# Performance work log

Measured on AMD Instinct MI355X. Metric: run time of the kernel, lower is better.

Reference implementation:

```python
import jax, jax.numpy as jnp
import numpy as np

N, NFEAT, NHID, NHEADS, NCLASS = 4096, 1024, 128, 8, 64
ALPHA = 0.2  # LeakyReLU negative slope
NEG_INF = -9e15


def setup_inputs() -> dict:
    key = jax.random.key(0)
    ks = jax.random.split(key, 8)
    x = jax.random.normal(ks[0], (N, NFEAT), dtype=jnp.float32)
    adj = jax.random.randint(ks[1], (N, N), 0, 2, dtype=jnp.int32)
    sW = 1.0 / np.sqrt(NFEAT)
    W = jax.random.normal(ks[2], (NHEADS, NFEAT, NHID), dtype=jnp.float32) * sW
    a1 = jax.random.normal(ks[3], (NHEADS, NHID), dtype=jnp.float32) * 0.1
    a2 = jax.random.normal(ks[4], (NHEADS, NHID), dtype=jnp.float32) * 0.1
    sWo = 1.0 / np.sqrt(NHID * NHEADS)
    Wo = jax.random.normal(ks[5], (NHID * NHEADS, NCLASS), dtype=jnp.float32) * sWo
    ao1 = jax.random.normal(ks[6], (NCLASS,), dtype=jnp.float32) * 0.1
    ao2 = jax.random.normal(ks[7], (NCLASS,), dtype=jnp.float32) * 0.1
    return {"x": x, "adj": adj, "W": W, "a1": a1, "a2": a2,
            "Wo": Wo, "ao1": ao1, "ao2": ao2}


def reference(x, adj, W, a1, a2, Wo, ao1, ao2):
    mask = adj > 0  # [N, N]
    # --- multi-head attention layer (concat=True) ---
    Wh = jnp.einsum('nf,hfd->hnd', x, W)            # [H, N, D]
    f1 = jnp.einsum('hnd,hd->hn', Wh, a1)           # [H, N] self score
    f2 = jnp.einsum('hnd,hd->hn', Wh, a2)           # [H, N] neighbor score
    e = jax.nn.leaky_relu(f1[:, :, None] + f2[:, None, :], negative_slope=ALPHA)
    e = jnp.where(mask[None, :, :], e, NEG_INF)
    attn = jax.nn.softmax(e, axis=-1)               # [H, N, N]
    h = jnp.einsum('hnm,hmd->hnd', attn, Wh)        # [H, N, D]
    h = jax.nn.elu(h)                               # concat=True applies elu
    h = jnp.transpose(h, (1, 0, 2)).reshape(N, NHEADS * NHID)  # concat heads
    # --- output attention layer (concat=False) ---
    Who = h @ Wo                                    # [N, C]
    g1 = Who @ ao1                                  # [N]
    g2 = Who @ ao2                                  # [N]
    eo = jax.nn.leaky_relu(g1[:, None] + g2[None, :], negative_slope=ALPHA)
    eo = jnp.where(mask, eo, NEG_INF)
    ao = jax.nn.softmax(eo, axis=-1)                # [N, N]
    out = ao @ Who                                  # [N, C]
    out = jax.nn.elu(out)                           # F.elu in GAT.forward
    return jax.nn.log_softmax(out, axis=1)
```

## Files before the change

### kernel.cpp

```cpp
#include <hip/hip_runtime.h>
#include <hip/hip_bf16.h>


#define NN    4096
#define NF    1024
#define DH    128
#define NHEADS 8
#define NCLS  64
#define ALPHA 0.2f
#define LOG2E 1.44269504f

using short8 = __attribute__((ext_vector_type(8))) short;
using f32x4  = __attribute__((ext_vector_type(4))) float;
using int4v  = __attribute__((ext_vector_type(4))) int;

static __device__ __forceinline__ float bf2f(unsigned short h) {
    return __uint_as_float(((unsigned int)h) << 16);
}
static __device__ __forceinline__ unsigned short f2bf(float f) {
    unsigned int u = __float_as_uint(f);
    u = (u + 0x7fffu + ((u >> 16) & 1u)) >> 16;
    return (unsigned short)u;
}
static __device__ __forceinline__ float fast_exp2(float x) {
    return __builtin_amdgcn_exp2f(x);
}

__global__ __launch_bounds__(256) void diag_fill(
    float* __restrict__ out, int n, float val)
{
    int i = blockIdx.x * 256 + threadIdx.x;
    if (i < n) out[i] = val;
}

__global__ __launch_bounds__(256) void convert_misc(
    const float* __restrict__ x, const float* __restrict__ a1,
    const float* __restrict__ a2, const float* __restrict__ ao1,
    const float* __restrict__ ao2, unsigned short* __restrict__ xB,
    unsigned short* __restrict__ a1B, unsigned short* __restrict__ a2B,
    unsigned short* __restrict__ ao1B, unsigned short* __restrict__ ao2B)
{
    int b = blockIdx.x, t = threadIdx.x;
    if (b < 4096) {
        long i = ((long)b * 256 + t) * 4;
        float4 v = *(const float4*)&x[i];
        unsigned u0 = (unsigned)f2bf(v.x) | ((unsigned)f2bf(v.y) << 16);
        unsigned u1 = (unsigned)f2bf(v.z) | ((unsigned)f2bf(v.w) << 16);
        uint2 u; u.x = u0; u.y = u1;
        *(uint2*)&xB[i] = u;
    } else if (b == 4096) {
        for (int i = t; i < NHEADS * DH; i += 256) {
            a1B[i] = f2bf(a1[i]);
            a2B[i] = f2bf(a2[i]);
        }
    } else {
        if (t < NCLS) {
            ao1B[t] = f2bf(ao1[t]);
            ao2B[t] = f2bf(ao2[t]);
        }
    }
}

__global__ __launch_bounds__(256) void transpose_cvt(
    const float* __restrict__ W, const float* __restrict__ Wo,
    unsigned short* __restrict__ WT, unsigned short* __restrict__ WoT)
{
    __shared__ unsigned short tile[32][33];
    int z = blockIdx.z;
    const float* in; unsigned short* out; int C;
    if (z < 8) { in = W + (long)z * NF * DH; out = WT + (long)z * DH * NF; C = DH; }
    else       { in = Wo;                    out = WoT;                    C = NCLS; }
    int x0 = blockIdx.x * 32, y0 = blockIdx.y * 32;
    if (x0 >= C) return;
    int t = threadIdx.x, tx = t & 31, ty = t >> 5;
    for (int yy = 0; yy < 32; yy += 8)
        tile[ty + yy][tx] = f2bf(in[(long)(y0 + ty + yy) * C + x0 + tx]);
    __syncthreads();
    for (int yy = 0; yy < 32; yy += 8)
        out[(long)(x0 + ty + yy) * NF + y0 + tx] = tile[tx][ty + yy];
}

__global__ __launch_bounds__(256) void build_mask(
    const int* __restrict__ adj, unsigned int* __restrict__ bm)
{
    long t4 = (long)blockIdx.x * 256 + threadIdx.x;
    int4v v = ((const int4v*)adj)[t4];
    unsigned nib = (v[0] > 0 ? 1u : 0u) | (v[1] > 0 ? 2u : 0u)
                 | (v[2] > 0 ? 4u : 0u) | (v[3] > 0 ? 8u : 0u);
    int l = threadIdx.x & 63;
    unsigned w = nib << (4 * (l & 7));
    w |= __shfl_xor(w, 1);
    w |= __shfl_xor(w, 2);
    w |= __shfl_xor(w, 4);
    if ((l & 7) == 0) bm[t4 >> 3] = w;
}

__global__ __launch_bounds__(256) void gemm_bt(
    const unsigned short* __restrict__ A, const unsigned short* __restrict__ Bt,
    unsigned short* __restrict__ Cc, int K, int Nn, long sAz, long sCz)
{
    __shared__ unsigned short Alds[64][72];
    __shared__ unsigned short Blds[128][72];
    int t = threadIdx.x;
    int w = t >> 6, l = t & 63;
    long aoff = (long)blockIdx.z * sAz + (long)blockIdx.y * 64 * K;
    long boff = (long)blockIdx.x * 128 * K;
    f32x4 acc[8];
#pragma unroll
    for (int i = 0; i < 8; ++i) acc[i] = (f32x4){0.f, 0.f, 0.f, 0.f};

    for (int k0 = 0; k0 < K; k0 += 64) {
#pragma unroll
        for (int it = 0; it < 2; ++it) {
            int ci = it * 256 + t;
            int r = ci >> 3, c8 = (ci & 7) * 8;
            *(short8*)&Alds[r][c8] = *(const short8*)&A[aoff + (long)r * K + k0 + c8];
        }
#pragma unroll
        for (int it = 0; it < 4; ++it) {
            int ci = it * 256 + t;
            int r = ci >> 3, c8 = (ci & 7) * 8;
            *(short8*)&Blds[r][c8] = *(const short8*)&Bt[boff + (long)r * K + k0 + c8];
        }
        __syncthreads();
        int arow = w * 16 + (l & 15);
        int koff = (l >> 4) * 8;
#pragma unroll
        for (int kc = 0; kc < 2; ++kc) {
            short8 af = *(const short8*)&Alds[arow][kc * 32 + koff];
#pragma unroll
            for (int dt = 0; dt < 8; ++dt) {
                short8 bf = *(const short8*)&Blds[dt * 16 + (l & 15)][kc * 32 + koff];
                acc[dt] = __builtin_amdgcn_mfma_f32_16x16x32_bf16(af, bf, acc[dt], 0, 0, 0);
            }
        }
        __syncthreads();
    }
    long coff = (long)blockIdx.z * sCz + ((long)blockIdx.y * 64) * Nn + blockIdx.x * 128;
    int mrow = w * 16 + (l >> 4) * 4;
#pragma unroll
    for (int dt = 0; dt < 8; ++dt) {
        int n = dt * 16 + (l & 15);
#pragma unroll
        for (int r = 0; r < 4; ++r)
            Cc[coff + (long)(mrow + r) * Nn + n] = f2bf(acc[dt][r]);
    }
}

__global__ __launch_bounds__(256) void gemm2_ks(
    const unsigned short* __restrict__ A, const unsigned short* __restrict__ Bt,
    float* __restrict__ accw, int K, int kchunk)
{
    __shared__ unsigned short Alds[64][72];
    __shared__ unsigned short Blds[128][72];
    int t = threadIdx.x;
    int w = t >> 6, l = t & 63;
    long boff = (long)blockIdx.x * 128 * K;
    int kz = blockIdx.z;
    f32x4 acc[8];
#pragma unroll
    for (int i = 0; i < 8; ++i) acc[i] = (f32x4){0.f, 0.f, 0.f, 0.f};

    for (int k0 = kz * kchunk; k0 < (kz + 1) * kchunk; k0 += 64) {
#pragma unroll
        for (int it = 0; it < 2; ++it) {
            int ci = it * 256 + t;
            int r = ci >> 3, c8 = (ci & 7) * 8;
            *(short8*)&Alds[r][c8] = *(const short8*)&A[(long)r * K + k0 + c8];
        }
#pragma unroll
        for (int it = 0; it < 4; ++it) {
            int ci = it * 256 + t;
            int r = ci >> 3, c8 = (ci & 7) * 8;
            *(short8*)&Blds[r][c8] = *(const short8*)&Bt[boff + (long)r * K + k0 + c8];
        }
        __syncthreads();
        int arow = w * 16 + (l & 15);
        int koff = (l >> 4) * 8;
#pragma unroll
        for (int kc = 0; kc < 2; ++kc) {
            short8 af = *(const short8*)&Alds[arow][kc * 32 + koff];
#pragma unroll
            for (int dt = 0; dt < 8; ++dt) {
                short8 bf = *(const short8*)&Blds[dt * 16 + (l & 15)][kc * 32 + koff];
                acc[dt] = __builtin_amdgcn_mfma_f32_16x16x32_bf16(af, bf, acc[dt], 0, 0, 0);
            }
        }
        __syncthreads();
    }
    int mrow = w * 16 + (l >> 4) * 4;
#pragma unroll
    for (int dt = 0; dt < 8; ++dt) {
        int n = blockIdx.x * 128 + dt * 16 + (l & 15);
        *(f32x4*)&accw[((long)kz * NN + n) * NCLS + mrow] = acc[dt];
    }
}

__global__ __launch_bounds__(256) void combinew(
    const float* __restrict__ accw, const unsigned short* __restrict__ ao1B,
    const unsigned short* __restrict__ ao2B, unsigned short* __restrict__ WhoT,
    float* __restrict__ g1, float* __restrict__ g2)
{
    int t = threadIdx.x, wv = t >> 6, l = t & 63;
    int n = blockIdx.x * 4 + wv;
    float v = 0.f;
#pragma unroll
    for (int kz = 0; kz < 4; ++kz)
        v += accw[((long)kz * NN + n) * NCLS + l];
    unsigned short b = f2bf(v);
    WhoT[(long)l * NN + n] = b;
    float vf = bf2f(b);
    float s1 = vf * bf2f(ao1B[l]);
    float s2 = vf * bf2f(ao2B[l]);
#pragma unroll
    for (int off = 32; off; off >>= 1) {
        s1 += __shfl_xor(s1, off);
        s2 += __shfl_xor(s2, off);
    }
    if (l == 0) { g1[n] = s1 * LOG2E; g2[n] = s2 * LOG2E; }
}

__global__ __launch_bounds__(256) void fscores(
    const unsigned short* __restrict__ T, const unsigned short* __restrict__ va,
    const unsigned short* __restrict__ vb, float* __restrict__ fa,
    float* __restrict__ fb, int D, int Nn)
{
    int h = blockIdx.y;
    int n = blockIdx.x * 256 + threadIdx.x;
    const unsigned short* Th = T + (long)h * D * Nn;
    float s1 = 0.f, s2 = 0.f;
    for (int d = 0; d < D; ++d) {
        float v = bf2f(Th[(long)d * Nn + n]);
        s1 += v * bf2f(va[h * D + d]);
        s2 += v * bf2f(vb[h * D + d]);
    }
    fa[h * Nn + n] = s1 * LOG2E;
    fb[h * Nn + n] = s2 * LOG2E;
}

static __device__ __forceinline__ float build_p16(
    unsigned int bits, float fi, const float* f2s, int pc0,
    short8& p0, short8& p1)
{
    float lsum = 0.f;
#pragma unroll
    for (int cc = 0; cc < 16; ++cc) {
        float wgt = 0.f;
        if ((bits >> cc) & 1u) {
            float e = fi + f2s[pc0 + cc];
            e = e > 0.f ? e : ALPHA * e;
            e = fminf(e, 60.f);
            wgt = fast_exp2(e);
        }
        unsigned short bw = f2bf(wgt);
        lsum += bf2f(bw);
        if (cc < 8) p0[cc] = (short)bw;
        else        p1[cc - 8] = (short)bw;
    }
    return lsum;
}

static __device__ __forceinline__ void build_pfrag3(
    unsigned long long wpair, float fi, const float* __restrict__ f2g,
    int kgrp, short8& a0, short8& a1)
{
    int4v av0, av1;
#pragma unroll
    for (int kc = 0; kc < 2; ++kc) {
        unsigned bits = (unsigned)(wpair >> (kc * 32 + kgrp * 8)) & 0xFFu;
        const float4* fp = (const float4*)(f2g + kc * 32 + kgrp * 8);
        float4 fv0 = fp[0], fv1 = fp[1];
        float ev[8] = {fv0.x, fv0.y, fv0.z, fv0.w, fv1.x, fv1.y, fv1.z, fv1.w};
#pragma unroll
        for (int jj = 0; jj < 8; jj += 2) {
            float e0 = fi + ev[jj], e1 = fi + ev[jj + 1];
            e0 = fmaxf(e0, ALPHA * e0);
            e1 = fmaxf(e1, ALPHA * e1);
            float w0 = fast_exp2(e0), w1 = fast_exp2(e1);
            w0 = ((bits >> jj) & 1u) ? w0 : 0.f;
            w1 = ((bits >> (jj + 1)) & 1u) ? w1 : 0.f;
            float2 fv; fv.x = w0; fv.y = w1;
            __hip_bfloat162 pk = __float22bfloat162_rn(fv);
            unsigned pu; __builtin_memcpy(&pu, &pk, 4);
            if (kc == 0) av0[jj >> 1] = (int)pu;
            else         av1[jj >> 1] = (int)pu;
        }
    }
    a0 = __builtin_bit_cast(short8, av0);
    a1 = __builtin_bit_cast(short8, av1);
}

__global__ __launch_bounds__(256) void attn1_direct(
    const float* __restrict__ f1, const float* __restrict__ f2,
    const unsigned int* __restrict__ bm, const unsigned short* __restrict__ WhT,
    unsigned short* __restrict__ hcat)
{
    __shared__ unsigned short Plds[64][72];
    __shared__ unsigned short Wlds[128][72];
    __shared__ float f1s[64], f2s[64], ssum[64][4], srow[64];
    int t = threadIdx.x;
    int h = blockIdx.y;
    int i0 = blockIdx.x * 64;
    int w = t >> 6, l = t & 63;
    if (t < 64) f1s[t] = f1[h * NN + i0 + t];
    f32x4 acc[8];
#pragma unroll
    for (int i = 0; i < 8; ++i) acc[i] = (f32x4){0.f, 0.f, 0.f, 0.f};
    float psum = 0.f;
    int pr = t >> 2, pc0 = (t & 3) * 16;
    const unsigned short* Wh_h = WhT + (long)h * DH * NN;

    for (int j0 = 0; j0 < NN; j0 += 64) {
        if (t < 64) f2s[t] = f2[h * NN + j0 + t];
        __syncthreads();
        {
            unsigned int word = bm[(long)(i0 + pr) * (NN / 32) + (j0 >> 5) + ((pc0 >> 5) & 1)];
            unsigned int bits = (word >> (pc0 & 16)) & 0xFFFFu;
            short8 p0, p1;
            psum += build_p16(bits, f1s[pr], f2s, pc0, p0, p1);
            *(short8*)&Plds[pr][pc0]     = p0;
            *(short8*)&Plds[pr][pc0 + 8] = p1;
        }
#pragma unroll
        for (int it = 0; it < 4; ++it) {
            int ci = it * 256 + t;
            int d = ci >> 3, c8 = (ci & 7) * 8;
            *(short8*)&Wlds[d][c8] = *(const short8*)&Wh_h[(long)d * NN + j0 + c8];
        }
        __syncthreads();
        int arow = w * 16 + (l & 15);
        int koff = (l >> 4) * 8;
#pragma unroll
        for (int kc = 0; kc < 2; ++kc) {
            short8 af = *(const short8*)&Plds[arow][kc * 32 + koff];
#pragma unroll
            for (int dt = 0; dt < 8; ++dt) {
                short8 bf = *(const short8*)&Wlds[dt * 16 + (l & 15)][kc * 32 + koff];
                acc[dt] = __builtin_amdgcn_mfma_f32_16x16x32_bf16(af, bf, acc[dt], 0, 0, 0);
            }
        }
        __syncthreads();
    }
    ssum[pr][t & 3] = psum;
    __syncthreads();
    if (t < 64) srow[t] = ssum[t][0] + ssum[t][1] + ssum[t][2] + ssum[t][3];
    __syncthreads();
    int mrow = w * 16 + (l >> 4) * 4;
#pragma unroll
    for (int dt = 0; dt < 8; ++dt) {
        int d = dt * 16 + (l & 15);
#pragma unroll
        for (int r = 0; r < 4; ++r) {
            float v = acc[dt][r] / fmaxf(srow[mrow + r], 1e-20f);
            v = v > 0.f ? v : __expf(v) - 1.f;
            hcat[(long)(i0 + mrow + r) * (NHEADS * DH) + h * DH + d] = f2bf(v);
        }
    }
}

__global__ __launch_bounds__(256) void attn1_part(
    const float* __restrict__ f1, const float* __restrict__ f2,
    const unsigned int* __restrict__ bm, const unsigned short* __restrict__ WhT,
    float* __restrict__ accp1, float* __restrict__ dsum1, int jspan)
{
    __shared__ unsigned short Wlds[128][72];
    int t = threadIdx.x;
    int h = blockIdx.y;
    int i0 = blockIdx.x * 64;
    int jz = blockIdx.z;
    int w = t >> 6, l = t & 63;
    int m = l & 15, kgrp = l >> 4;
    int myrow = i0 + w * 16 + m;
    float fi = f1[h * NN + myrow];
    const unsigned int* bmrow = bm + (long)myrow * (NN / 32);
    const float* f2h = f2 + (long)h * NN;
    const unsigned short* Wh_h = WhT + (long)h * DH * NN;
    short8 ones;
#pragma unroll
    for (int i = 0; i < 8; ++i) ones[i] = (short)0x3F80;
    f32x4 acc[8];
#pragma unroll
    for (int i = 0; i < 8; ++i) acc[i] = (f32x4){0.f, 0.f, 0.f, 0.f};
    f32x4 accd = (f32x4){0.f, 0.f, 0.f, 0.f};

    for (int j0 = jz * jspan; j0 < (jz + 1) * jspan; j0 += 64) {
        unsigned long long wpair;
        __builtin_memcpy(&wpair, &bmrow[j0 >> 5], 8);
#pragma unroll
        for (int it = 0; it < 4; ++it) {
            int ci = it * 256 + t;
            int d = ci >> 3, c8 = (ci & 7) * 8;
            *(short8*)&Wlds[d][c8] = *(const short8*)&Wh_h[(long)d * NN + j0 + c8];
        }
        short8 a0, a1;
        build_pfrag3(wpair, fi, f2h + j0, kgrp, a0, a1);
        __syncthreads();
        accd = __builtin_amdgcn_mfma_f32_16x16x32_bf16(a0, ones, accd, 0, 0, 0);
        accd = __builtin_amdgcn_mfma_f32_16x16x32_bf16(a1, ones, accd, 0, 0, 0);
#pragma unroll
        for (int dt = 0; dt < 8; ++dt) {
            short8 b0 = *(const short8*)&Wlds[dt * 16 + m][kgrp * 8];
            acc[dt] = __builtin_amdgcn_mfma_f32_16x16x32_bf16(a0, b0, acc[dt], 0, 0, 0);
        }
#pragma unroll
        for (int dt = 0; dt < 8; ++dt) {
            short8 b1 = *(const short8*)&Wlds[dt * 16 + m][32 + kgrp * 8];
            acc[dt] = __builtin_amdgcn_mfma_f32_16x16x32_bf16(a1, b1, acc[dt], 0, 0, 0);
        }
        __syncthreads();
    }
    if (m == 0) {
#pragma unroll
        for (int r = 0; r < 4; ++r)
            dsum1[((long)jz * NHEADS + h) * NN + i0 + w * 16 + kgrp * 4 + r] = accd[r];
    }
    int mrow = w * 16 + kgrp * 4;
#pragma unroll
    for (int dt = 0; dt < 8; ++dt) {
        int d = dt * 16 + m;
#pragma unroll
        for (int r = 0; r < 4; ++r)
            accp1[((long)jz * NN + i0 + mrow + r) * (NHEADS * DH) + h * DH + d] = acc[dt][r];
    }
}

__global__ __launch_bounds__(256) void combine1(
    const float* __restrict__ accp1, const float* __restrict__ dsum1,
    unsigned short* __restrict__ hcat, int js)
{
    long idx = (long)blockIdx.x * 256 + threadIdx.x;
    int i = (int)(idx >> 10), c = (int)(idx & 1023), h = c >> 7;
    float v = 0.f, s = 0.f;
    for (int jz = 0; jz < js; ++jz) {
        v += accp1[((long)jz * NN + i) * (NHEADS * DH) + c];
        s += dsum1[((long)jz * NHEADS + h) * NN + i];
    }
    v /= fmaxf(s, 1e-20f);
    v = v > 0.f ? v : __expf(v) - 1.f;
    hcat[idx] = f2bf(v);
}

__global__ __launch_bounds__(256) void attn2(
    const float* __restrict__ g1, const float* __restrict__ g2,
    const unsigned int* __restrict__ bm, const unsigned short* __restrict__ WhoT,
    float* __restrict__ accp, float* __restrict__ sp, int jspan)
{
    __shared__ unsigned short Wlds[64][72];
    int t = threadIdx.x;
    int i0 = blockIdx.x * 64;
    int jc = blockIdx.y;
    int w = t >> 6, l = t & 63;
    int m = l & 15, kgrp = l >> 4;
    int myrow = i0 + w * 16 + m;
    float fi = g1[myrow];
    const unsigned int* bmrow = bm + (long)myrow * (NN / 32);
    short8 ones;
#pragma unroll
    for (int i = 0; i < 8; ++i) ones[i] = (short)0x3F80;
    f32x4 acc[4];
#pragma unroll
    for (int i = 0; i < 4; ++i) acc[i] = (f32x4){0.f, 0.f, 0.f, 0.f};
    f32x4 accd = (f32x4){0.f, 0.f, 0.f, 0.f};

    for (int j0 = jc * jspan; j0 < (jc + 1) * jspan; j0 += 64) {
        unsigned long long wpair;
        __builtin_memcpy(&wpair, &bmrow[j0 >> 5], 8);
#pragma unroll
        for (int it = 0; it < 2; ++it) {
            int ci = it * 256 + t;
            int d = ci >> 3, c8 = (ci & 7) * 8;
            *(short8*)&Wlds[d][c8] = *(const short8*)&WhoT[(long)d * NN + j0 + c8];
        }
        short8 a0, a1;
        build_pfrag3(wpair, fi, g2 + j0, kgrp, a0, a1);
        __syncthreads();
        accd = __builtin_amdgcn_mfma_f32_16x16x32_bf16(a0, ones, accd, 0, 0, 0);
        accd = __builtin_amdgcn_mfma_f32_16x16x32_bf16(a1, ones, accd, 0, 0, 0);
#pragma unroll
        for (int dt = 0; dt < 4; ++dt) {
            short8 b0 = *(const short8*)&Wlds[dt * 16 + m][kgrp * 8];
            acc[dt] = __builtin_amdgcn_mfma_f32_16x16x32_bf16(a0, b0, acc[dt], 0, 0, 0);
        }
#pragma unroll
        for (int dt = 0; dt < 4; ++dt) {
            short8 b1 = *(const short8*)&Wlds[dt * 16 + m][32 + kgrp * 8];
            acc[dt] = __builtin_amdgcn_mfma_f32_16x16x32_bf16(a1, b1, acc[dt], 0, 0, 0);
        }
        __syncthreads();
    }
    if (m == 0) {
#pragma unroll
        for (int r = 0; r < 4; ++r)
            sp[(long)jc * NN + i0 + w * 16 + kgrp * 4 + r] = accd[r];
    }
    int mrow = w * 16 + kgrp * 4;
#pragma unroll
    for (int dt = 0; dt < 4; ++dt) {
        int d = dt * 16 + m;
#pragma unroll
        for (int r = 0; r < 4; ++r)
            accp[((long)jc * NN + i0 + mrow + r) * NCLS + d] = acc[dt][r];
    }
}

__global__ __launch_bounds__(256) void finalize(
    const float* __restrict__ accp, const float* __restrict__ sp,
    float* __restrict__ out, int js)
{
    int t = threadIdx.x;
    int wv = t >> 6, l = t & 63;
    int r = blockIdx.x * 4 + wv;
    float v = 0.f, s = 0.f;
    for (int jc = 0; jc < js; ++jc) {
        v += accp[((long)jc * NN + r) * NCLS + l];
        s += sp[(long)jc * NN + r];
    }
    v /= fmaxf(s, 1e-20f);
    v = v > 0.f ? v : __expf(v) - 1.f;
    float m = v;
#pragma unroll
    for (int off = 32; off; off >>= 1) m = fmaxf(m, __shfl_xor(m, off));
    float ex = __expf(v - m);
#pragma unroll
    for (int off = 32; off; off >>= 1) ex += __shfl_xor(ex, off);
    out[(long)r * NCLS + l] = v - (m + __logf(ex));
}

extern "C" void kernel_launch(void* const* d_in, const int* in_sizes, int n_in,
                              void* d_out, int out_size, void* d_ws, size_t ws_size,
                              hipStream_t stream)
{
    const float* x   = (const float*)d_in[0];
    const int*   adj = (const int*)d_in[1];
    const float* W   = (const float*)d_in[2];
    const float* a1  = (const float*)d_in[3];
    const float* a2  = (const float*)d_in[4];
    const float* Wo  = (const float*)d_in[5];
    const float* ao1 = (const float*)d_in[6];
    const float* ao2 = (const float*)d_in[7];
    float* out = (float*)d_out;

    const long SZ_XB   = (long)NN * NF * 2;
    const long SZ_AB   = (long)NHEADS * DH * 2;
    const long SZ_AOB  = (long)NCLS * 2;
    const long SZ_WT   = (long)NHEADS * DH * NF * 2;
    const long SZ_WOT  = (long)NCLS * NF * 2;
    const long SZ_WHT  = (long)NHEADS * DH * NN * 2;
    const long SZ_HCAT = (long)NN * NHEADS * DH * 2;
    const long SZ_WHOT = (long)NCLS * NN * 2;
    const long SZ_F    = (long)NHEADS * NN * 4;
    const long SZ_G    = (long)NN * 4;
    const long SZ_BM   = (long)NN * (NN / 32) * 4;
    const long SZ_ACW  = (long)4 * NN * NCLS * 4;
    const long SZ_AP1  = (long)NN * NHEADS * DH * 4;
    const long SZ_DS1  = (long)NHEADS * NN * 4;
    const long SZ_AP2  = (long)NN * NCLS * 4;
    const long SZ_SP2  = (long)NN * 4;
    long base = SZ_XB + 2 * SZ_AB + 2 * SZ_AOB + SZ_WT + SZ_WOT + SZ_WHT
              + SZ_HCAT + SZ_WHOT + 2 * SZ_F + 2 * SZ_G + SZ_BM + SZ_ACW
              + 40 * 256;

    int js1, js2;
    if ((size_t)(base + 4 * (SZ_AP1 + SZ_DS1) + 16 * (SZ_AP2 + SZ_SP2)) <= ws_size) {
        js1 = 4; js2 = 16;
    } else if ((size_t)(base + 4 * (SZ_AP1 + SZ_DS1) + 8 * (SZ_AP2 + SZ_SP2)) <= ws_size) {
        js1 = 4; js2 = 8;
    } else if ((size_t)(base + 2 * (SZ_AP1 + SZ_DS1) + 8 * (SZ_AP2 + SZ_SP2)) <= ws_size) {
        js1 = 2; js2 = 8;
    } else if ((size_t)(base + 16 * (SZ_AP2 + SZ_SP2)) <= ws_size) {
        js1 = 1; js2 = 16;
    } else if ((size_t)(base + 4 * (SZ_AP2 + SZ_SP2)) <= ws_size) {
        js1 = 1; js2 = 4;
    } else {
        diag_fill<<<dim3((out_size + 255) / 256), 256, 0, stream>>>(
            out, out_size, (float)(ws_size >> 20));
        return;
    }

    char* p = (char*)d_ws;
    auto alloc = [&](long bytes) { char* q = p; p += (bytes + 255) & ~255L; return q; };
    unsigned short* xB   = (unsigned short*)alloc(SZ_XB);
    unsigned short* a1B  = (unsigned short*)alloc(SZ_AB);
    unsigned short* a2B  = (unsigned short*)alloc(SZ_AB);
    unsigned short* ao1B = (unsigned short*)alloc(SZ_AOB);
    unsigned short* ao2B = (unsigned short*)alloc(SZ_AOB);
    unsigned short* WT   = (unsigned short*)alloc(SZ_WT);
    unsigned short* WoT  = (unsigned short*)alloc(SZ_WOT);
    unsigned short* WhT  = (unsigned short*)alloc(SZ_WHT);
    unsigned short* hcat = (unsigned short*)alloc(SZ_HCAT);
    unsigned short* WhoT = (unsigned short*)alloc(SZ_WHOT);
    float* f1 = (float*)alloc(SZ_F);
    float* f2 = (float*)alloc(SZ_F);
    float* g1 = (float*)alloc(SZ_G);
    float* g2 = (float*)alloc(SZ_G);
    unsigned int* bm = (unsigned int*)alloc(SZ_BM);
    float* accw  = (float*)alloc(SZ_ACW);
    float* accp2 = (float*)alloc(js2 * SZ_AP2);
    float* sp2   = (float*)alloc(js2 * SZ_SP2);
    float* accp1 = (float*)(js1 > 1 ? alloc(js1 * SZ_AP1) : nullptr);
    float* dsum1 = (float*)(js1 > 1 ? alloc(js1 * SZ_DS1) : nullptr);

    convert_misc<<<dim3(4098), 256, 0, stream>>>(
        x, a1, a2, ao1, ao2, xB, a1B, a2B, ao1B, ao2B);
    transpose_cvt<<<dim3(4, NF / 32, 9), 256, 0, stream>>>(W, Wo, WT, WoT);
    build_mask<<<dim3((int)(((long)NN * NN) / 1024)), 256, 0, stream>>>(adj, bm);
    gemm_bt<<<dim3(NN / 128, DH / 64, NHEADS), 256, 0, stream>>>(
        WT, xB, WhT, NF, NN, (long)DH * NF, (long)DH * NN);
    fscores<<<dim3(NN / 256, NHEADS), 256, 0, stream>>>(WhT, a1B, a2B, f1, f2, DH, NN);
    if (js1 > 1) {
        attn1_part<<<dim3(NN / 64, NHEADS, js1), 256, 0, stream>>>(
            f1, f2, bm, WhT, accp1, dsum1, NN / js1);
        combine1<<<dim3((int)(((long)NN * NHEADS * DH) / 256)), 256, 0, stream>>>(
            accp1, dsum1, hcat, js1);
    } else {
        attn1_direct<<<dim3(NN / 64, NHEADS), 256, 0, stream>>>(f1, f2, bm, WhT, hcat);
    }
    gemm2_ks<<<dim3(NN / 128, 1, 4), 256, 0, stream>>>(WoT, hcat, accw, NF, NF / 4);
    combinew<<<dim3(NN / 4), 256, 0, stream>>>(accw, ao1B, ao2B, WhoT, g1, g2);
    attn2<<<dim3(NN / 64, js2), 256, 0, stream>>>(g1, g2, bm, WhoT, accp2, sp2, NN / js2);
    finalize<<<dim3(NN / 4), 256, 0, stream>>>(accp2, sp2, out, js2);
}
```

Before: 340.3 us.

## Process two row tiles per block in attention kernels and vectorize combine

attn1_part and attn2 now handle 128 rows per block instead of 64. Each wave builds two probability fragments and reuses every shared-memory V tile for both, which halves LDS staging and global loads of Wh per row processed. combine1 is vectorized to read float4 partials and write four bf16 values per thread. The cost is doubled accumulator registers, which may lower occupancy, and half as many blocks in the attention grids.

```diff
diff --git a/kernel.cpp b/kernel.cpp
--- a/kernel.cpp
+++ b/kernel.cpp
@@ -366,61 +366,78 @@
     __shared__ unsigned short Wlds[128][72];
     int t = threadIdx.x;
     int h = blockIdx.y;
-    int i0 = blockIdx.x * 64;
+    int i0 = blockIdx.x * 128;
     int jz = blockIdx.z;
     int w = t >> 6, l = t & 63;
     int m = l & 15, kgrp = l >> 4;
-    int myrow = i0 + w * 16 + m;
-    float fi = f1[h * NN + myrow];
-    const unsigned int* bmrow = bm + (long)myrow * (NN / 32);
+    int rowA = i0 + w * 16 + m;
+    int rowB = rowA + 64;
+    float fiA = f1[h * NN + rowA];
+    float fiB = f1[h * NN + rowB];
+    const unsigned int* bmA = bm + (long)rowA * (NN / 32);
+    const unsigned int* bmB = bm + (long)rowB * (NN / 32);
     const float* f2h = f2 + (long)h * NN;
     const unsigned short* Wh_h = WhT + (long)h * DH * NN;
     short8 ones;
 #pragma unroll
     for (int i = 0; i < 8; ++i) ones[i] = (short)0x3F80;
-    f32x4 acc[8];
-#pragma unroll
-    for (int i = 0; i < 8; ++i) acc[i] = (f32x4){0.f, 0.f, 0.f, 0.f};
-    f32x4 accd = (f32x4){0.f, 0.f, 0.f, 0.f};
+    f32x4 accA[8], accB[8];
+#pragma unroll
+    for (int i = 0; i < 8; ++i) {
+        accA[i] = (f32x4){0.f, 0.f, 0.f, 0.f};
+        accB[i] = (f32x4){0.f, 0.f, 0.f, 0.f};
+    }
+    f32x4 accdA = (f32x4){0.f, 0.f, 0.f, 0.f};
+    f32x4 accdB = (f32x4){0.f, 0.f, 0.f, 0.f};
 
     for (int j0 = jz * jspan; j0 < (jz + 1) * jspan; j0 += 64) {
-        unsigned long long wpair;
-        __builtin_memcpy(&wpair, &bmrow[j0 >> 5], 8);
+        unsigned long long wpA, wpB;
+        __builtin_memcpy(&wpA, &bmA[j0 >> 5], 8);
+        __builtin_memcpy(&wpB, &bmB[j0 >> 5], 8);
 #pragma unroll
         for (int it = 0; it < 4; ++it) {
             int ci = it * 256 + t;
             int d = ci >> 3, c8 = (ci & 7) * 8;
             *(short8*)&Wlds[d][c8] = *(const short8*)&Wh_h[(long)d * NN + j0 + c8];
         }
-        short8 a0, a1;
-        build_pfrag3(wpair, fi, f2h + j0, kgrp, a0, a1);
-        __syncthreads();
-        accd = __builtin_amdgcn_mfma_f32_16x16x32_bf16(a0, ones, accd, 0, 0, 0);
-        accd = __builtin_amdgcn_mfma_f32_16x16x32_bf16(a1, ones, accd, 0, 0, 0);
+        short8 a0A, a1A, a0B, a1B;
+        build_pfrag3(wpA, fiA, f2h + j0, kgrp, a0A, a1A);
+        build_pfrag3(wpB, fiB, f2h + j0, kgrp, a0B, a1B);
+        __syncthreads();
+        accdA = __builtin_amdgcn_mfma_f32_16x16x32_bf16(a0A, ones, accdA, 0, 0, 0);
+        accdA = __builtin_amdgcn_mfma_f32_16x16x32_bf16(a1A, ones, accdA, 0, 0, 0);
+        accdB = __builtin_amdgcn_mfma_f32_16x16x32_bf16(a0B, ones, accdB, 0, 0, 0);
+        accdB = __builtin_amdgcn_mfma_f32_16x16x32_bf16(a1B, ones, accdB, 0, 0, 0);
 #pragma unroll
         for (int dt = 0; dt < 8; ++dt) {
             short8 b0 = *(const short8*)&Wlds[dt * 16 + m][kgrp * 8];
-            acc[dt] = __builtin_amdgcn_mfma_f32_16x16x32_bf16(a0, b0, acc[dt], 0, 0, 0);
+            accA[dt] = __builtin_amdgcn_mfma_f32_16x16x32_bf16(a0A, b0, accA[dt], 0, 0, 0);
+            accB[dt] = __builtin_amdgcn_mfma_f32_16x16x32_bf16(a0B, b0, accB[dt], 0, 0, 0);
         }
 #pragma unroll
         for (int dt = 0; dt < 8; ++dt) {
             short8 b1 = *(const short8*)&Wlds[dt * 16 + m][32 + kgrp * 8];
-            acc[dt] = __builtin_amdgcn_mfma_f32_16x16x32_bf16(a1, b1, acc[dt], 0, 0, 0);
+            accA[dt] = __builtin_amdgcn_mfma_f32_16x16x32_bf16(a1A, b1, accA[dt], 0, 0, 0);
+            accB[dt] = __builtin_amdgcn_mfma_f32_16x16x32_bf16(a1B, b1, accB[dt], 0, 0, 0);
         }
         __syncthreads();
     }
     if (m == 0) {
 #pragma unroll
-        for (int r = 0; r < 4; ++r)
-            dsum1[((long)jz * NHEADS + h) * NN + i0 + w * 16 + kgrp * 4 + r] = accd[r];
+        for (int r = 0; r < 4; ++r) {
+            dsum1[((long)jz * NHEADS + h) * NN + i0 + w * 16 + kgrp * 4 + r]      = accdA[r];
+            dsum1[((long)jz * NHEADS + h) * NN + i0 + 64 + w * 16 + kgrp * 4 + r] = accdB[r];
+        }
     }
     int mrow = w * 16 + kgrp * 4;
 #pragma unroll
     for (int dt = 0; dt < 8; ++dt) {
         int d = dt * 16 + m;
 #pragma unroll
-        for (int r = 0; r < 4; ++r)
-            accp1[((long)jz * NN + i0 + mrow + r) * (NHEADS * DH) + h * DH + d] = acc[dt][r];
+        for (int r = 0; r < 4; ++r) {
+            accp1[((long)jz * NN + i0 + mrow + r) * (NHEADS * DH) + h * DH + d]      = accA[dt][r];
+            accp1[((long)jz * NN + i0 + 64 + mrow + r) * (NHEADS * DH) + h * DH + d] = accB[dt][r];
+        }
     }
 }
 
@@ -428,16 +445,23 @@
     const float* __restrict__ accp1, const float* __restrict__ dsum1,
     unsigned short* __restrict__ hcat, int js)
 {
-    long idx = (long)blockIdx.x * 256 + threadIdx.x;
-    int i = (int)(idx >> 10), c = (int)(idx & 1023), h = c >> 7;
-    float v = 0.f, s = 0.f;
+    long idx4 = (long)blockIdx.x * 256 + threadIdx.x;
+    int i = (int)(idx4 >> 8), c4 = (int)(idx4 & 255) * 4, h = c4 >> 7;
+    float4 v = {0.f, 0.f, 0.f, 0.f};
+    float s = 0.f;
     for (int jz = 0; jz < js; ++jz) {
-        v += accp1[((long)jz * NN + i) * (NHEADS * DH) + c];
+        float4 pv = *(const float4*)&accp1[((long)jz * NN + i) * (NHEADS * DH) + c4];
+        v.x += pv.x; v.y += pv.y; v.z += pv.z; v.w += pv.w;
         s += dsum1[((long)jz * NHEADS + h) * NN + i];
     }
-    v /= fmaxf(s, 1e-20f);
-    v = v > 0.f ? v : __expf(v) - 1.f;
-    hcat[idx] = f2bf(v);
+    float inv = 1.f / fmaxf(s, 1e-20f);
+    float o[4] = {v.x * inv, v.y * inv, v.z * inv, v.w * inv};
+#pragma unroll
+    for (int k = 0; k < 4; ++k) o[k] = o[k] > 0.f ? o[k] : __expf(o[k]) - 1.f;
+    unsigned u0 = (unsigned)f2bf(o[0]) | ((unsigned)f2bf(o[1]) << 16);
+    unsigned u1 = (unsigned)f2bf(o[2]) | ((unsigned)f2bf(o[3]) << 16);
+    uint2 u; u.x = u0; u.y = u1;
+    *(uint2*)&hcat[(long)i * (NHEADS * DH) + c4] = u;
 }
 
 __global__ __launch_bounds__(256) void attn2(
@@ -447,59 +471,75 @@
 {
     __shared__ unsigned short Wlds[64][72];
     int t = threadIdx.x;
-    int i0 = blockIdx.x * 64;
+    int i0 = blockIdx.x * 128;
     int jc = blockIdx.y;
     int w = t >> 6, l = t & 63;
     int m = l & 15, kgrp = l >> 4;
-    int myrow = i0 + w * 16 + m;
-    float fi = g1[myrow];
-    const unsigned int* bmrow = bm + (long)myrow * (NN / 32);
+    int rowA = i0 + w * 16 + m;
+    int rowB = rowA + 64;
+    float fiA = g1[rowA], fiB = g1[rowB];
+    const unsigned int* bmA = bm + (long)rowA * (NN / 32);
+    const unsigned int* bmB = bm + (long)rowB * (NN / 32);
     short8 ones;
 #pragma unroll
     for (int i = 0; i < 8; ++i) ones[i] = (short)0x3F80;
-    f32x4 acc[4];
-#pragma unroll
-    for (int i = 0; i < 4; ++i) acc[i] = (f32x4){0.f, 0.f, 0.f, 0.f};
-    f32x4 accd = (f32x4){0.f, 0.f, 0.f, 0.f};
+    f32x4 accA[4], accB[4];
+#pragma unroll
+    for (int i = 0; i < 4; ++i) {
+        accA[i] = (f32x4){0.f, 0.f, 0.f, 0.f};
+        accB[i] = (f32x4){0.f, 0.f, 0.f, 0.f};
+    }
+    f32x4 accdA = (f32x4){0.f, 0.f, 0.f, 0.f};
+    f32x4 accdB = (f32x4){0.f, 0.f, 0.f, 0.f};
 
     for (int j0 = jc * jspan; j0 < (jc + 1) * jspan; j0 += 64) {
-        unsigned long long wpair;
-        __builtin_memcpy(&wpair, &bmrow[j0 >> 5], 8);
+        unsigned long long wpA, wpB;
+        __builtin_memcpy(&wpA, &bmA[j0 >> 5], 8);
+        __builtin_memcpy(&wpB, &bmB[j0 >> 5], 8);
 #pragma unroll
         for (int it = 0; it < 2; ++it) {
             int ci = it * 256 + t;
             int d = ci >> 3, c8 = (ci & 7) * 8;
             *(short8*)&Wlds[d][c8] = *(const short8*)&WhoT[(long)d * NN + j0 + c8];
         }
-        short8 a0, a1;
-        build_pfrag3(wpair, fi, g2 + j0, kgrp, a0, a1);
-        __syncthreads();
-        accd = __builtin_amdgcn_mfma_f32_16x16x32_bf16(a0, ones, accd, 0, 0, 0);
-        accd = __builtin_amdgcn_mfma_f32_16x16x32_bf16(a1, ones, accd, 0, 0, 0);
+        short8 a0A, a1A, a0B, a1B;
+        build_pfrag3(wpA, fiA, g2 + j0, kgrp, a0A, a1A);
+        build_pfrag3(wpB, fiB, g2 + j0, kgrp, a0B, a1B);
+        __syncthreads();
+        accdA = __builtin_amdgcn_mfma_f32_16x16x32_bf16(a0A, ones, accdA, 0, 0, 0);
+        accdA = __builtin_amdgcn_mfma_f32_16x16x32_bf16(a1A, ones, accdA, 0, 0, 0);
+        accdB = __builtin_amdgcn_mfma_f32_16x16x32_bf16(a0B, ones, accdB, 0, 0, 0);
+        accdB = __builtin_amdgcn_mfma_f32_16x16x32_bf16(a1B, ones, accdB, 0, 0, 0);
 #pragma unroll
         for (int dt = 0; dt < 4; ++dt) {
             short8 b0 = *(const short8*)&Wlds[dt * 16 + m][kgrp * 8];
-            acc[dt] = __builtin_amdgcn_mfma_f32_16x16x32_bf16(a0, b0, acc[dt], 0, 0, 0);
+            accA[dt] = __builtin_amdgcn_mfma_f32_16x16x32_bf16(a0A, b0, accA[dt], 0, 0, 0);
+            accB[dt] = __builtin_amdgcn_mfma_f32_16x16x32_bf16(a0B, b0, accB[dt], 0, 0, 0);
         }
 #pragma unroll
         for (int dt = 0; dt < 4; ++dt) {
             short8 b1 = *(const short8*)&Wlds[dt * 16 + m][32 + kgrp * 8];
-            acc[dt] = __builtin_amdgcn_mfma_f32_16x16x32_bf16(a1, b1, acc[dt], 0, 0, 0);
+            accA[dt] = __builtin_amdgcn_mfma_f32_16x16x32_bf16(a1A, b1, accA[dt], 0, 0, 0);
+            accB[dt] = __builtin_amdgcn_mfma_f32_16x16x32_bf16(a1B, b1, accB[dt], 0, 0, 0);
         }
         __syncthreads();
     }
     if (m == 0) {
 #pragma unroll
-        for (int r = 0; r < 4; ++r)
-            sp[(long)jc * NN + i0 + w * 16 + kgrp * 4 + r] = accd[r];
+        for (int r = 0; r < 4; ++r) {
+            sp[(long)jc * NN + i0 + w * 16 + kgrp * 4 + r]      = accdA[r];
+            sp[(long)jc * NN + i0 + 64 + w * 16 + kgrp * 4 + r] = accdB[r];
+        }
     }
     int mrow = w * 16 + kgrp * 4;
 #pragma unroll
     for (int dt = 0; dt < 4; ++dt) {
         int d = dt * 16 + m;
 #pragma unroll
-        for (int r = 0; r < 4; ++r)
-            accp[((long)jc * NN + i0 + mrow + r) * NCLS + d] = acc[dt][r];
+        for (int r = 0; r < 4; ++r) {
+            accp[((long)jc * NN + i0 + mrow + r) * NCLS + d]      = accA[dt][r];
+            accp[((long)jc * NN + i0 + 64 + mrow + r) * NCLS + d] = accB[dt][r];
+        }
     }
 }
 
@@ -608,15 +648,15 @@
         WT, xB, WhT, NF, NN, (long)DH * NF, (long)DH * NN);
     fscores<<<dim3(NN / 256, NHEADS), 256, 0, stream>>>(WhT, a1B, a2B, f1, f2, DH, NN);
     if (js1 > 1) {
-        attn1_part<<<dim3(NN / 64, NHEADS, js1), 256, 0, stream>>>(
+        attn1_part<<<dim3(NN / 128, NHEADS, js1), 256, 0, stream>>>(
             f1, f2, bm, WhT, accp1, dsum1, NN / js1);
-        combine1<<<dim3((int)(((long)NN * NHEADS * DH) / 256)), 256, 0, stream>>>(
+        combine1<<<dim3((int)(((long)NN * NHEADS * DH) / 1024)), 256, 0, stream>>>(
             accp1, dsum1, hcat, js1);
     } else {
         attn1_direct<<<dim3(NN / 64, NHEADS), 256, 0, stream>>>(f1, f2, bm, WhT, hcat);
     }
     gemm2_ks<<<dim3(NN / 128, 1, 4), 256, 0, stream>>>(WoT, hcat, accw, NF, NF / 4);
     combinew<<<dim3(NN / 4), 256, 0, stream>>>(accw, ao1B, ao2B, WhoT, g1, g2);
-    attn2<<<dim3(NN / 64, js2), 256, 0, stream>>>(g1, g2, bm, WhoT, accp2, sp2, NN / js2);
+    attn2<<<dim3(NN / 128, js2), 256, 0, stream>>>(g1, g2, bm, WhoT, accp2, sp2, NN / js2);
     finalize<<<dim3(NN / 4), 256, 0, stream>>>(accp2, sp2, out, js2);
 }
```

New measurement: 353.5 us. 1.04x slower.

## Fuse preprocessing kernels and fold attention scores into GEMM epilogues

Applied to the files above, without the earlier changes.

Merges the bf16 conversion, weight transposes and adjacency bitmask build into one prep launch. The f1/f2 score reduction moves into the first GEMM's epilogue through shared and global atomics, which needs a memset first. The split-K second GEMM and its combine pass become a single non-split GEMM that also writes g1/g2. combine1 is vectorised to float4. The aim is fewer launches and less intermediate traffic, at the cost of atomics and lower parallelism in the second GEMM.

```diff
diff --git a/kernel.cpp b/kernel.cpp
--- a/kernel.cpp
+++ b/kernel.cpp
@@ -33,22 +33,53 @@
     if (i < n) out[i] = val;
 }
 
-__global__ __launch_bounds__(256) void convert_misc(
-    const float* __restrict__ x, const float* __restrict__ a1,
-    const float* __restrict__ a2, const float* __restrict__ ao1,
-    const float* __restrict__ ao2, unsigned short* __restrict__ xB,
+__global__ __launch_bounds__(256) void prep(
+    const float* __restrict__ x, const int* __restrict__ adj,
+    const float* __restrict__ W, const float* __restrict__ Wo,
+    const float* __restrict__ a1, const float* __restrict__ a2,
+    const float* __restrict__ ao1, const float* __restrict__ ao2,
+    unsigned short* __restrict__ xB, unsigned int* __restrict__ bm,
+    unsigned short* __restrict__ WT, unsigned short* __restrict__ WoT,
     unsigned short* __restrict__ a1B, unsigned short* __restrict__ a2B,
     unsigned short* __restrict__ ao1B, unsigned short* __restrict__ ao2B)
 {
+    __shared__ unsigned short tile[32][33];
     int b = blockIdx.x, t = threadIdx.x;
-    if (b < 4096) {
-        long i = ((long)b * 256 + t) * 4;
+    if (b < 16384) {
+        long t4 = (long)b * 256 + t;
+        int4v v = ((const int4v*)adj)[t4];
+        unsigned nib = (v[0] > 0 ? 1u : 0u) | (v[1] > 0 ? 2u : 0u)
+                     | (v[2] > 0 ? 4u : 0u) | (v[3] > 0 ? 8u : 0u);
+        int l = t & 63;
+        unsigned w = nib << (4 * (l & 7));
+        w |= __shfl_xor(w, 1);
+        w |= __shfl_xor(w, 2);
+        w |= __shfl_xor(w, 4);
+        if ((l & 7) == 0) bm[t4 >> 3] = w;
+    } else if (b < 20480) {
+        long i = ((long)(b - 16384) * 256 + t) * 4;
         float4 v = *(const float4*)&x[i];
         unsigned u0 = (unsigned)f2bf(v.x) | ((unsigned)f2bf(v.y) << 16);
         unsigned u1 = (unsigned)f2bf(v.z) | ((unsigned)f2bf(v.w) << 16);
         uint2 u; u.x = u0; u.y = u1;
         *(uint2*)&xB[i] = u;
-    } else if (b == 4096) {
+    } else if (b < 21632) {
+        int tid = b - 20480;
+        int z = tid >> 7;
+        int rem = tid & 127;
+        int bx = rem & 3, by = rem >> 2;
+        const float* in; unsigned short* out; int C;
+        if (z < 8) { in = W + (long)z * NF * DH; out = WT + (long)z * DH * NF; C = DH; }
+        else       { in = Wo;                    out = WoT;                    C = NCLS; }
+        int x0 = bx * 32, y0 = by * 32;
+        if (x0 >= C) return;
+        int tx = t & 31, ty = t >> 5;
+        for (int yy = 0; yy < 32; yy += 8)
+            tile[ty + yy][tx] = f2bf(in[(long)(y0 + ty + yy) * C + x0 + tx]);
+        __syncthreads();
+        for (int yy = 0; yy < 32; yy += 8)
+            out[(long)(x0 + ty + yy) * NF + y0 + tx] = tile[tx][ty + yy];
+    } else if (b == 21632) {
         for (int i = t; i < NHEADS * DH; i += 256) {
             a1B[i] = f2bf(a1[i]);
             a2B[i] = f2bf(a2[i]);
@@ -61,66 +92,37 @@
     }
 }
 
-__global__ __launch_bounds__(256) void transpose_cvt(
-    const float* __restrict__ W, const float* __restrict__ Wo,
-    unsigned short* __restrict__ WT, unsigned short* __restrict__ WoT)
-{
-    __shared__ unsigned short tile[32][33];
-    int z = blockIdx.z;
-    const float* in; unsigned short* out; int C;
-    if (z < 8) { in = W + (long)z * NF * DH; out = WT + (long)z * DH * NF; C = DH; }
-    else       { in = Wo;                    out = WoT;                    C = NCLS; }
-    int x0 = blockIdx.x * 32, y0 = blockIdx.y * 32;
-    if (x0 >= C) return;
-    int t = threadIdx.x, tx = t & 31, ty = t >> 5;
-    for (int yy = 0; yy < 32; yy += 8)
-        tile[ty + yy][tx] = f2bf(in[(long)(y0 + ty + yy) * C + x0 + tx]);
-    __syncthreads();
-    for (int yy = 0; yy < 32; yy += 8)
-        out[(long)(x0 + ty + yy) * NF + y0 + tx] = tile[tx][ty + yy];
-}
-
-__global__ __launch_bounds__(256) void build_mask(
-    const int* __restrict__ adj, unsigned int* __restrict__ bm)
-{
-    long t4 = (long)blockIdx.x * 256 + threadIdx.x;
-    int4v v = ((const int4v*)adj)[t4];
-    unsigned nib = (v[0] > 0 ? 1u : 0u) | (v[1] > 0 ? 2u : 0u)
-                 | (v[2] > 0 ? 4u : 0u) | (v[3] > 0 ? 8u : 0u);
-    int l = threadIdx.x & 63;
-    unsigned w = nib << (4 * (l & 7));
-    w |= __shfl_xor(w, 1);
-    w |= __shfl_xor(w, 2);
-    w |= __shfl_xor(w, 4);
-    if ((l & 7) == 0) bm[t4 >> 3] = w;
-}
-
-__global__ __launch_bounds__(256) void gemm_bt(
+__global__ __launch_bounds__(256) void gemm1_fs(
     const unsigned short* __restrict__ A, const unsigned short* __restrict__ Bt,
-    unsigned short* __restrict__ Cc, int K, int Nn, long sAz, long sCz)
+    unsigned short* __restrict__ Cc, const unsigned short* __restrict__ a1B,
+    const unsigned short* __restrict__ a2B, float* __restrict__ f1,
+    float* __restrict__ f2)
 {
     __shared__ unsigned short Alds[64][72];
     __shared__ unsigned short Blds[128][72];
+    __shared__ float s1l[128], s2l[128];
     int t = threadIdx.x;
     int w = t >> 6, l = t & 63;
-    long aoff = (long)blockIdx.z * sAz + (long)blockIdx.y * 64 * K;
-    long boff = (long)blockIdx.x * 128 * K;
+    int h = blockIdx.z;
+    long aoff = (long)h * DH * NF + (long)blockIdx.y * 64 * NF;
+    long boff = (long)blockIdx.x * 128 * NF;
+    if (t < 128) { s1l[t] = 0.f; s2l[t] = 0.f; }
     f32x4 acc[8];
 #pragma unroll
     for (int i = 0; i < 8; ++i) acc[i] = (f32x4){0.f, 0.f, 0.f, 0.f};
 
-    for (int k0 = 0; k0 < K; k0 += 64) {
+    for (int k0 = 0; k0 < NF; k0 += 64) {
 #pragma unroll
         for (int it = 0; it < 2; ++it) {
             int ci = it * 256 + t;
             int r = ci >> 3, c8 = (ci & 7) * 8;
-            *(short8*)&Alds[r][c8] = *(const short8*)&A[aoff + (long)r * K + k0 + c8];
+            *(short8*)&Alds[r][c8] = *(const short8*)&A[aoff + (long)r * NF + k0 + c8];
         }
 #pragma unroll
         for (int it = 0; it < 4; ++it) {
             int ci = it * 256 + t;
             int r = ci >> 3, c8 = (ci & 7) * 8;
-            *(short8*)&Blds[r][c8] = *(const short8*)&Bt[boff + (long)r * K + k0 + c8];
+            *(short8*)&Blds[r][c8] = *(const short8*)&Bt[boff + (long)r * NF + k0 + c8];
         }
         __syncthreads();
         int arow = w * 16 + (l & 15);
@@ -136,43 +138,61 @@
         }
         __syncthreads();
     }
-    long coff = (long)blockIdx.z * sCz + ((long)blockIdx.y * 64) * Nn + blockIdx.x * 128;
+    long coff = (long)h * DH * NN + ((long)blockIdx.y * 64) * NN + blockIdx.x * 128;
     int mrow = w * 16 + (l >> 4) * 4;
+    int dbase = blockIdx.y * 64;
 #pragma unroll
     for (int dt = 0; dt < 8; ++dt) {
         int n = dt * 16 + (l & 15);
-#pragma unroll
-        for (int r = 0; r < 4; ++r)
-            Cc[coff + (long)(mrow + r) * Nn + n] = f2bf(acc[dt][r]);
-    }
-}
-
-__global__ __launch_bounds__(256) void gemm2_ks(
+        float p1 = 0.f, p2 = 0.f;
+#pragma unroll
+        for (int r = 0; r < 4; ++r) {
+            unsigned short bw = f2bf(acc[dt][r]);
+            Cc[coff + (long)(mrow + r) * NN + n] = bw;
+            float vf = bf2f(bw);
+            int d = dbase + mrow + r;
+            p1 += vf * bf2f(a1B[h * DH + d]);
+            p2 += vf * bf2f(a2B[h * DH + d]);
+        }
+        atomicAdd(&s1l[n], p1);
+        atomicAdd(&s2l[n], p2);
+    }
+    __syncthreads();
+    if (t < 128) {
+        int n = blockIdx.x * 128 + t;
+        atomicAdd(&f1[h * NN + n], s1l[t] * LOG2E);
+        atomicAdd(&f2[h * NN + n], s2l[t] * LOG2E);
+    }
+}
+
+__global__ __launch_bounds__(256) void gemm2c(
     const unsigned short* __restrict__ A, const unsigned short* __restrict__ Bt,
-    float* __restrict__ accw, int K, int kchunk)
+    const unsigned short* __restrict__ ao1B, const unsigned short* __restrict__ ao2B,
+    unsigned short* __restrict__ WhoT, float* __restrict__ g1, float* __restrict__ g2)
 {
     __shared__ unsigned short Alds[64][72];
-    __shared__ unsigned short Blds[128][72];
+    __shared__ unsigned short Blds[64][72];
+    __shared__ float s1l[64], s2l[64];
     int t = threadIdx.x;
     int w = t >> 6, l = t & 63;
-    long boff = (long)blockIdx.x * 128 * K;
-    int kz = blockIdx.z;
-    f32x4 acc[8];
-#pragma unroll
-    for (int i = 0; i < 8; ++i) acc[i] = (f32x4){0.f, 0.f, 0.f, 0.f};
-
-    for (int k0 = kz * kchunk; k0 < (kz + 1) * kchunk; k0 += 64) {
+    int n0 = blockIdx.x * 64;
+    if (t < 64) { s1l[t] = 0.f; s2l[t] = 0.f; }
+    f32x4 acc[4];
+#pragma unroll
+    for (int i = 0; i < 4; ++i) acc[i] = (f32x4){0.f, 0.f, 0.f, 0.f};
+
+    for (int k0 = 0; k0 < NF; k0 += 64) {
 #pragma unroll
         for (int it = 0; it < 2; ++it) {
             int ci = it * 256 + t;
             int r = ci >> 3, c8 = (ci & 7) * 8;
-            *(short8*)&Alds[r][c8] = *(const short8*)&A[(long)r * K + k0 + c8];
-        }
-#pragma unroll
-        for (int it = 0; it < 4; ++it) {
+            *(short8*)&Alds[r][c8] = *(const short8*)&A[(long)r * NF + k0 + c8];
+        }
+#pragma unroll
+        for (int it = 0; it < 2; ++it) {
             int ci = it * 256 + t;
             int r = ci >> 3, c8 = (ci & 7) * 8;
-            *(short8*)&Blds[r][c8] = *(const short8*)&Bt[boff + (long)r * K + k0 + c8];
+            *(short8*)&Blds[r][c8] = *(const short8*)&Bt[(long)(n0 + r) * NF + k0 + c8];
         }
         __syncthreads();
         int arow = w * 16 + (l & 15);
@@ -181,7 +201,7 @@
         for (int kc = 0; kc < 2; ++kc) {
             short8 af = *(const short8*)&Alds[arow][kc * 32 + koff];
 #pragma unroll
-            for (int dt = 0; dt < 8; ++dt) {
+            for (int dt = 0; dt < 4; ++dt) {
                 short8 bf = *(const short8*)&Blds[dt * 16 + (l & 15)][kc * 32 + koff];
                 acc[dt] = __builtin_amdgcn_mfma_f32_16x16x32_bf16(af, bf, acc[dt], 0, 0, 0);
             }
@@ -190,52 +210,26 @@
     }
     int mrow = w * 16 + (l >> 4) * 4;
 #pragma unroll
-    for (int dt = 0; dt < 8; ++dt) {
-        int n = blockIdx.x * 128 + dt * 16 + (l & 15);
-        *(f32x4*)&accw[((long)kz * NN + n) * NCLS + mrow] = acc[dt];
-    }
-}
-
-__global__ __launch_bounds__(256) void combinew(
-    const float* __restrict__ accw, const unsigned short* __restrict__ ao1B,
-    const unsigned short* __restrict__ ao2B, unsigned short* __restrict__ WhoT,
-    float* __restrict__ g1, float* __restrict__ g2)
-{
-    int t = threadIdx.x, wv = t >> 6, l = t & 63;
-    int n = blockIdx.x * 4 + wv;
-    float v = 0.f;
-#pragma unroll
-    for (int kz = 0; kz < 4; ++kz)
-        v += accw[((long)kz * NN + n) * NCLS + l];
-    unsigned short b = f2bf(v);
-    WhoT[(long)l * NN + n] = b;
-    float vf = bf2f(b);
-    float s1 = vf * bf2f(ao1B[l]);
-    float s2 = vf * bf2f(ao2B[l]);
-#pragma unroll
-    for (int off = 32; off; off >>= 1) {
-        s1 += __shfl_xor(s1, off);
-        s2 += __shfl_xor(s2, off);
-    }
-    if (l == 0) { g1[n] = s1 * LOG2E; g2[n] = s2 * LOG2E; }
-}
-
-__global__ __launch_bounds__(256) void fscores(
-    const unsigned short* __restrict__ T, const unsigned short* __restrict__ va,
-    const unsigned short* __restrict__ vb, float* __restrict__ fa,
-    float* __restrict__ fb, int D, int Nn)
-{
-    int h = blockIdx.y;
-    int n = blockIdx.x * 256 + threadIdx.x;
-    const unsigned short* Th = T + (long)h * D * Nn;
-    float s1 = 0.f, s2 = 0.f;
-    for (int d = 0; d < D; ++d) {
-        float v = bf2f(Th[(long)d * Nn + n]);
-        s1 += v * bf2f(va[h * D + d]);
-        s2 += v * bf2f(vb[h * D + d]);
-    }
-    fa[h * Nn + n] = s1 * LOG2E;
-    fb[h * Nn + n] = s2 * LOG2E;
+    for (int dt = 0; dt < 4; ++dt) {
+        int nl = dt * 16 + (l & 15);
+        float p1 = 0.f, p2 = 0.f;
+#pragma unroll
+        for (int r = 0; r < 4; ++r) {
+            int c = mrow + r;
+            unsigned short bw = f2bf(acc[dt][r]);
+            WhoT[(long)c * NN + n0 + nl] = bw;
+            float vf = bf2f(bw);
+            p1 += vf * bf2f(ao1B[c]);
+            p2 += vf * bf2f(ao2B[c]);
+        }
+        atomicAdd(&s1l[nl], p1);
+        atomicAdd(&s2l[nl], p2);
+    }
+    __syncthreads();
+    if (t < 64) {
+        g1[n0 + t] = s1l[t] * LOG2E;
+        g2[n0 + t] = s2l[t] * LOG2E;
+    }
 }
 
 static __device__ __forceinline__ float build_p16(
@@ -428,16 +422,23 @@
     const float* __restrict__ accp1, const float* __restrict__ dsum1,
     unsigned short* __restrict__ hcat, int js)
 {
-    long idx = (long)blockIdx.x * 256 + threadIdx.x;
-    int i = (int)(idx >> 10), c = (int)(idx & 1023), h = c >> 7;
-    float v = 0.f, s = 0.f;
+    long idx4 = (long)blockIdx.x * 256 + threadIdx.x;
+    int i = (int)(idx4 >> 8), c4 = (int)(idx4 & 255) * 4, h = c4 >> 7;
+    float4 v = {0.f, 0.f, 0.f, 0.f};
+    float s = 0.f;
     for (int jz = 0; jz < js; ++jz) {
-        v += accp1[((long)jz * NN + i) * (NHEADS * DH) + c];
+        float4 pv = *(const float4*)&accp1[((long)jz * NN + i) * (NHEADS * DH) + c4];
+        v.x += pv.x; v.y += pv.y; v.z += pv.z; v.w += pv.w;
         s += dsum1[((long)jz * NHEADS + h) * NN + i];
     }
-    v /= fmaxf(s, 1e-20f);
-    v = v > 0.f ? v : __expf(v) - 1.f;
-    hcat[idx] = f2bf(v);
+    float inv = 1.f / fmaxf(s, 1e-20f);
+    float o[4] = {v.x * inv, v.y * inv, v.z * inv, v.w * inv};
+#pragma unroll
+    for (int k = 0; k < 4; ++k) o[k] = o[k] > 0.f ? o[k] : __expf(o[k]) - 1.f;
+    unsigned u0 = (unsigned)f2bf(o[0]) | ((unsigned)f2bf(o[1]) << 16);
+    unsigned u1 = (unsigned)f2bf(o[2]) | ((unsigned)f2bf(o[3]) << 16);
+    uint2 u; u.x = u0; u.y = u1;
+    *(uint2*)&hcat[(long)i * (NHEADS * DH) + c4] = u;
 }
 
 __global__ __launch_bounds__(256) void attn2(
@@ -551,13 +552,12 @@
     const long SZ_F    = (long)NHEADS * NN * 4;
     const long SZ_G    = (long)NN * 4;
     const long SZ_BM   = (long)NN * (NN / 32) * 4;
-    const long SZ_ACW  = (long)4 * NN * NCLS * 4;
     const long SZ_AP1  = (long)NN * NHEADS * DH * 4;
     const long SZ_DS1  = (long)NHEADS * NN * 4;
     const long SZ_AP2  = (long)NN * NCLS * 4;
     const long SZ_SP2  = (long)NN * 4;
     long base = SZ_XB + 2 * SZ_AB + 2 * SZ_AOB + SZ_WT + SZ_WOT + SZ_WHT
-              + SZ_HCAT + SZ_WHOT + 2 * SZ_F + 2 * SZ_G + SZ_BM + SZ_ACW
+              + SZ_HCAT + SZ_WHOT + 2 * SZ_F + 2 * SZ_G + SZ_BM
               + 40 * 256;
 
     int js1, js2;
@@ -594,29 +594,26 @@
     float* g1 = (float*)alloc(SZ_G);
     float* g2 = (float*)alloc(SZ_G);
     unsigned int* bm = (unsigned int*)alloc(SZ_BM);
-    float* accw  = (float*)alloc(SZ_ACW);
     float* accp2 = (float*)alloc(js2 * SZ_AP2);
     float* sp2   = (float*)alloc(js2 * SZ_SP2);
     float* accp1 = (float*)(js1 > 1 ? alloc(js1 * SZ_AP1) : nullptr);
     float* dsum1 = (float*)(js1 > 1 ? alloc(js1 * SZ_DS1) : nullptr);
 
-    convert_misc<<<dim3(4098), 256, 0, stream>>>(
-        x, a1, a2, ao1, ao2, xB, a1B, a2B, ao1B, ao2B);
-    transpose_cvt<<<dim3(4, NF / 32, 9), 256, 0, stream>>>(W, Wo, WT, WoT);
-    build_mask<<<dim3((int)(((long)NN * NN) / 1024)), 256, 0, stream>>>(adj, bm);
-    gemm_bt<<<dim3(NN / 128, DH / 64, NHEADS), 256, 0, stream>>>(
-        WT, xB, WhT, NF, NN, (long)DH * NF, (long)DH * NN);
-    fscores<<<dim3(NN / 256, NHEADS), 256, 0, stream>>>(WhT, a1B, a2B, f1, f2, DH, NN);
+    hipMemsetAsync(f1, 0, 2 * SZ_F, stream);
+    prep<<<dim3(21634), 256, 0, stream>>>(
+        x, adj, W, Wo, a1, a2, ao1, ao2,
+        xB, bm, WT, WoT, a1B, a2B, ao1B, ao2B);
+    gemm1_fs<<<dim3(NN / 128, DH / 64, NHEADS), 256, 0, stream>>>(
+        WT, xB, WhT, a1B, a2B, f1, f2);
     if (js1 > 1) {
         attn1_part<<<dim3(NN / 64, NHEADS, js1), 256, 0, stream>>>(
             f1, f2, bm, WhT, accp1, dsum1, NN / js1);
-        combine1<<<dim3((int)(((long)NN * NHEADS * DH) / 256)), 256, 0, stream>>>(
+        combine1<<<dim3((int)(((long)NN * NHEADS * DH) / 1024)), 256, 0, stream>>>(
             accp1, dsum1, hcat, js1);
     } else {
         attn1_direct<<<dim3(NN / 64, NHEADS), 256, 0, stream>>>(f1, f2, bm, WhT, hcat);
     }
-    gemm2_ks<<<dim3(NN / 128, 1, 4), 256, 0, stream>>>(WoT, hcat, accw, NF, NF / 4);
-    combinew<<<dim3(NN / 4), 256, 0, stream>>>(accw, ao1B, ao2B, WhoT, g1, g2);
+    gemm2c<<<dim3(NN / 64), 256, 0, stream>>>(WoT, hcat, ao1B, ao2B, WhoT, g1, g2);
     attn2<<<dim3(NN / 64, js2), 256, 0, stream>>>(g1, g2, bm, WhoT, accp2, sp2, NN / js2);
     finalize<<<dim3(NN / 4), 256, 0, stream>>>(accp2, sp2, out, js2);
 }
```

After: 306.7 us. 1.11x faster.
